# Kernel tuning notes

Measured on AMD Instinct MI355X. Metric: run time of the kernel, lower is better.

## Reference

```python
import jax, jax.numpy as jnp
import numpy as np

N = 100000        # nodes
E_RAND = 1600000  # random edges (self loops appended -> E = E_RAND + N)
H = 64            # agg_hidden
IN = 7            # in_channels
L = 3             # n_layer
FC = 128          # fc_hidden
C = 2             # num_classes
G = 256           # graphs in the batch
SLOPE = 0.2       # GATv2 LeakyReLU negative slope


def _gatv2(x, src, dst, Wl, bl, Wr, br, att, bias):
    # GATv2Conv, heads=1, concat=True, no edge_attr
    xl = x @ Wl.T + bl                                      # [N,H] source transform
    xr = x @ Wr.T + br                                      # [N,H] target transform
    e = jax.nn.leaky_relu(xl[src] + xr[dst], SLOPE) @ att   # [E] per-edge score
    m = jax.ops.segment_max(e, dst, num_segments=N)         # segment softmax over in-edges
    w = jnp.exp(e - m[dst])
    denom = jax.ops.segment_sum(w, dst, num_segments=N)
    alpha = w / denom[dst]                                  # self loops guarantee denom > 0
    out = jax.ops.segment_sum(alpha[:, None] * xl[src], dst, num_segments=N)
    return out + bias


def _forward(x, eps, m0, v0, mrest, vrest, fc1_W, fc1_b, fc2_W, fc2_b, edge_index, batch):
    src, dst = edge_index[0], edge_index[1]
    mean = jax.nn.elu(_gatv2(x, src, dst, *m0))
    log_var = jax.nn.elu(_gatv2(x, src, dst, *v0))
    for i in range(L - 1):  # dropout is a no-op in eval mode
        mean = jax.nn.elu(_gatv2(mean, src, dst, *[p[i] for p in mrest]))
        log_var = jax.nn.elu(_gatv2(log_var, src, dst, *[p[i] for p in vrest]))
    z = mean + eps * jnp.exp(0.5 * log_var)                 # reparameterize
    counts = jax.ops.segment_sum(jnp.ones((N,), z.dtype), batch, num_segments=G)
    zg = jax.ops.segment_sum(z, batch, num_segments=G) / counts[:, None]  # global_mean_pool
    h = jax.nn.relu(zg @ fc1_W.T + fc1_b)
    logits = h @ fc2_W.T + fc2_b
    return jax.nn.log_softmax(logits, axis=1), mean, log_var


def setup_inputs() -> dict:
    key = jax.random.key(0)
    ks = iter(jax.random.split(key, 48))

    def nrm(shape, s=0.1):
        return s * jax.random.normal(next(ks), shape, jnp.float32)

    x = jax.random.normal(next(ks), (N, IN), jnp.float32)
    src = jax.random.randint(next(ks), (E_RAND,), 0, N)
    dst = jax.random.randint(next(ks), (E_RAND,), 0, N)
    loops = jnp.arange(N)
    edge_index = jnp.stack([jnp.concatenate([src, loops]),
                            jnp.concatenate([dst, loops])])  # add_self_loops=True
    batch = jnp.sort(jax.random.randint(next(ks), (N,), 0, G))
    eps = jax.random.normal(next(ks), (N, H), jnp.float32)

    d = dict(x=x, eps=eps, edge_index=edge_index, batch=batch)
    for pre, din in (("m0", IN), ("v0", IN)):
        d[pre + "_Wl"] = nrm((H, din)); d[pre + "_bl"] = nrm((H,))
        d[pre + "_Wr"] = nrm((H, din)); d[pre + "_br"] = nrm((H,))
        d[pre + "_att"] = nrm((H,));    d[pre + "_bias"] = nrm((H,))
    for pre in ("m", "v"):  # stacked hidden layers [L-1, ...]
        d[pre + "_Wl"] = nrm((L - 1, H, H)); d[pre + "_bl"] = nrm((L - 1, H))
        d[pre + "_Wr"] = nrm((L - 1, H, H)); d[pre + "_br"] = nrm((L - 1, H))
        d[pre + "_att"] = nrm((L - 1, H));   d[pre + "_bias"] = nrm((L - 1, H))
    d["fc1_W"] = nrm((FC, H)); d["fc1_b"] = nrm((FC,))
    d["fc2_W"] = nrm((C, FC)); d["fc2_b"] = nrm((C,))
    return d


def reference(x, eps, edge_index, batch,
              m0_Wl, m0_bl, m0_Wr, m0_br, m0_att, m0_bias,
              v0_Wl, v0_bl, v0_Wr, v0_br, v0_att, v0_bias,
              m_Wl, m_bl, m_Wr, m_br, m_att, m_bias,
              v_Wl, v_bl, v_Wr, v_br, v_att, v_bias,
              fc1_W, fc1_b, fc2_W, fc2_b):
    m0 = (m0_Wl, m0_bl, m0_Wr, m0_br, m0_att, m0_bias)
    v0 = (v0_Wl, v0_bl, v0_Wr, v0_br, v0_att, v0_bias)
    mrest = (m_Wl, m_bl, m_Wr, m_br, m_att, m_bias)
    vrest = (v_Wl, v_bl, v_Wr, v_br, v_att, v_bias)
    return _forward(x, eps, m0, v0, mrest, vrest, fc1_W, fc1_b, fc2_W, fc2_b, edge_index, batch)
```

## Files before the change

### kernel.cpp

```cpp
#include <hip/hip_runtime.h>
#include <hip/hip_fp16.h>
#include <math.h>


#define BSH 7
#define BMSK ((1 << BSH) - 1)
#define CHUNK 4096
#define SNB 4096

typedef _Float16 h2 __attribute__((ext_vector_type(2)));
typedef _Float16 h8 __attribute__((ext_vector_type(8)));
typedef float f4 __attribute__((ext_vector_type(4)));

__device__ __forceinline__ float elu1(float v) {
    return v > 0.f ? v : (__expf(v) - 1.f);
}

__device__ __forceinline__ float exp2fast(float x) {
#if defined(__has_builtin)
#if __has_builtin(__builtin_amdgcn_exp2f)
    return __builtin_amdgcn_exp2f(x);
#else
    return exp2f(x);
#endif
#else
    return exp2f(x);
#endif
}

__device__ __forceinline__ float dot2f(h2 a, h2 b, float c) {
#if defined(__has_builtin)
#if __has_builtin(__builtin_amdgcn_fdot2)
    return __builtin_amdgcn_fdot2(a, b, c, false);
#else
    return fmaf((float)a.x, (float)b.x, fmaf((float)a.y, (float)b.y, c));
#endif
#else
    return fmaf((float)a.x, (float)b.x, fmaf((float)a.y, (float)b.y, c));
#endif
}

template <int CTRL>
__device__ __forceinline__ float dppf(float v) {
    int r = __builtin_amdgcn_update_dpp(0, __builtin_bit_cast(int, v), CTRL, 0xF, 0xF, true);
    return __builtin_bit_cast(float, r);
}


__global__ void k_hist_bucket(const int* __restrict__ dst, int E,
                              int* __restrict__ bcnt, int nbk) {
    __shared__ int h[1024];
    for (int i = threadIdx.x; i < 1024; i += blockDim.x) h[i] = 0;
    __syncthreads();
    int stride = gridDim.x * blockDim.x;
    for (int e = blockIdx.x * blockDim.x + threadIdx.x; e < E; e += stride)
        atomicAdd(&h[dst[e] >> BSH], 1);
    __syncthreads();
    for (int i = threadIdx.x; i < nbk; i += blockDim.x)
        if (h[i]) atomicAdd(&bcnt[i], h[i]);
}

__global__ void k_scan_buckets(const int* __restrict__ bcnt, int nbk, int* __restrict__ boff,
                               int* __restrict__ bfill, int* __restrict__ bin_cnt) {
    __shared__ int sh[1024];
    int t = threadIdx.x;
    if (t < nbk) bfill[t] = 0;
    if (t < 256) bin_cnt[t] = 0;
    int v = (t < nbk) ? bcnt[t] : 0;
    sh[t] = v;
    __syncthreads();
    for (int o = 1; o < 1024; o <<= 1) {
        int u = (t >= o) ? sh[t - o] : 0;
        __syncthreads();
        sh[t] += u;
        __syncthreads();
    }
    if (t < nbk) boff[t] = sh[t] - v;
    if (t == nbk - 1) boff[nbk] = sh[t];
}

__global__ __launch_bounds__(256) void k_binfill(
    const int* __restrict__ src, const int* __restrict__ dst, int E,
    const int* __restrict__ boff, int* __restrict__ bfill, int* __restrict__ pairs) {
    __shared__ int h[1024];
    __shared__ int sbase[1024];
    int c0 = blockIdx.x * CHUNK;
    int c1 = min(c0 + CHUNK, E);
    for (int i = threadIdx.x; i < 1024; i += 256) h[i] = 0;
    __syncthreads();
    for (int e = c0 + threadIdx.x; e < c1; e += 256)
        atomicAdd(&h[dst[e] >> BSH], 1);
    __syncthreads();
    for (int i = threadIdx.x; i < 1024; i += 256) {
        int c = h[i];
        sbase[i] = c ? (boff[i] + atomicAdd(&bfill[i], c)) : 0;
        h[i] = 0;
    }
    __syncthreads();
    for (int e = c0 + threadIdx.x; e < c1; e += 256) {
        int d = dst[e];
        int b = d >> BSH;
        int off = atomicAdd(&h[b], 1);
        pairs[sbase[b] + off] = (src[e] << BSH) | (d & BMSK);
    }
}

__global__ __launch_bounds__(256) void k_bucket_csr(
    const int* __restrict__ pairs, const int* __restrict__ boff,
    int* __restrict__ rowptr, int* __restrict__ col, int N, int E) {
    __shared__ int deg[128], fill[128], scan[128], base[128];
    int b = blockIdx.x;
    int e0 = boff[b], e1 = boff[b + 1];
    int t = threadIdx.x;
    if (t < 128) { deg[t] = 0; fill[t] = 0; }
    __syncthreads();
    for (int i = e0 + t; i < e1; i += 256)
        atomicAdd(&deg[pairs[i] & BMSK], 1);
    __syncthreads();
    if (t < 128) scan[t] = deg[t];
    __syncthreads();
    for (int o = 1; o < 128; o <<= 1) {
        int u = (t >= o && t < 128) ? scan[t - o] : 0;
        __syncthreads();
        if (t < 128) scan[t] += u;
        __syncthreads();
    }
    if (t < 128) {
        int excl = e0 + scan[t] - deg[t];
        int node = (b << BSH) + t;
        if (node < N) rowptr[node] = excl;
        if (node == N - 1) rowptr[N] = E;
        base[t] = excl;
    }
    __syncthreads();
    for (int i = e0 + t; i < e1; i += 256) {
        int pk = pairs[i];
        int d = pk & BMSK;
        int pos = base[d] + atomicAdd(&fill[d], 1);
        col[pos] = ((unsigned)pk) >> BSH;
    }
}


__global__ __launch_bounds__(256) void k_deg_hist(const int* __restrict__ rowptr, int n,
                                                  int* __restrict__ bin_cnt,
                                                  int* __restrict__ blk_base) {
    __shared__ int h[256];
    h[threadIdx.x] = 0;
    __syncthreads();
    int b0 = blockIdx.x * SNB;
    int b1 = min(b0 + SNB, n);
    for (int i = b0 + threadIdx.x; i < b1; i += 256) {
        int d = 255 - min(rowptr[i + 1] - rowptr[i], 255);
        atomicAdd(&h[d], 1);
    }
    __syncthreads();
    int c = h[threadIdx.x];
    blk_base[blockIdx.x * 256 + threadIdx.x] = c ? atomicAdd(&bin_cnt[threadIdx.x], c) : 0;
}

__global__ void k_scan256(const int* __restrict__ bin_cnt, int* __restrict__ bin_off,
                          float* __restrict__ zsum, int G) {
    __shared__ int sh[256];
    int t = threadIdx.x;
    for (int i = t; i < G * 64; i += 256) zsum[i] = 0.f;
    int v = bin_cnt[t];
    sh[t] = v;
    __syncthreads();
    for (int o = 1; o < 256; o <<= 1) {
        int u = (t >= o) ? sh[t - o] : 0;
        __syncthreads();
        sh[t] += u;
        __syncthreads();
    }
    bin_off[t] = sh[t] - v;
}

__global__ __launch_bounds__(256) void k_deg_scatter(const int* __restrict__ rowptr, int n,
                                                     const int* __restrict__ bin_off,
                                                     const int* __restrict__ blk_base,
                                                     int* __restrict__ nodeof) {
    __shared__ int h[256];
    h[threadIdx.x] = 0;
    __syncthreads();
    int b0 = blockIdx.x * SNB;
    int b1 = min(b0 + SNB, n);
    for (int i = b0 + threadIdx.x; i < b1; i += 256) {
        int d = 255 - min(rowptr[i + 1] - rowptr[i], 255);
        int my = atomicAdd(&h[d], 1);
        nodeof[bin_off[d] + blk_base[blockIdx.x * 256 + d] + my] = i;
    }
}


__global__ void k_transform7(const float* __restrict__ X,
                             const float* __restrict__ mWl, const float* __restrict__ mbl,
                             const float* __restrict__ mWr, const float* __restrict__ mbr,
                             const float* __restrict__ vWl, const float* __restrict__ vbl,
                             const float* __restrict__ vWr, const float* __restrict__ vbr,
                             __half* __restrict__ xlb, __half* __restrict__ xrb, int n) {
    int t = blockIdx.x * blockDim.x + threadIdx.x;
    int node = t >> 6;
    if (node >= n) return;
    int h = t & 63;
    float aml = mbl[h], amr = mbr[h], avl = vbl[h], avr = vbr[h];
#pragma unroll
    for (int k = 0; k < 7; ++k) {
        float xv = X[node * 7 + k];
        aml = fmaf(xv, mWl[h * 7 + k], aml);
        amr = fmaf(xv, mWr[h * 7 + k], amr);
        avl = fmaf(xv, vWl[h * 7 + k], avl);
        avr = fmaf(xv, vWr[h * 7 + k], avr);
    }
    size_t o = (size_t)node * 128;
    xlb[o + h] = __float2half(aml);
    xlb[o + 64 + h] = __float2half(avl);
    xrb[o + h] = __float2half(amr);
    xrb[o + 64 + h] = __float2half(avr);
}

__global__ __launch_bounds__(256) void k_transform_mfma2(
    const __half* __restrict__ Xm, const __half* __restrict__ Xv,
    const float* __restrict__ mWl, const float* __restrict__ mbl,
    const float* __restrict__ mWr, const float* __restrict__ mbr,
    const float* __restrict__ vWl, const float* __restrict__ vbl,
    const float* __restrict__ vWr, const float* __restrict__ vbr,
    __half* __restrict__ xlb, __half* __restrict__ xrb, int n) {
    int brn = blockIdx.y;
    const __half* X = brn ? Xv : Xm;
    const float* Wl = brn ? vWl : mWl;
    const float* bl = brn ? vbl : mbl;
    const float* Wr = brn ? vWr : mWr;
    const float* br = brn ? vbr : mbr;
    int base = brn * 64;

    __shared__ float biasLds[128];
    {
        int t = threadIdx.x;
        if (t < 64) biasLds[t] = bl[t];
        else if (t < 128) biasLds[t] = br[t - 64];
    }
    __syncthreads();
    int lane = threadIdx.x & 63;
    int l16 = lane & 15, lhi = lane >> 4;

    h8 aW[2][8];
    const float* Wp0 = Wl + (size_t)l16 * 64 + lhi * 8;
    const float* Wp1 = Wr + (size_t)l16 * 64 + lhi * 8;
#pragma unroll
    for (int tl = 0; tl < 4; ++tl) {
#pragma unroll
        for (int c = 0; c < 2; ++c) {
            const float* p0 = Wp0 + (size_t)tl * 16 * 64 + c * 32;
            const float* p1 = Wp1 + (size_t)tl * 16 * 64 + c * 32;
            float4 u0 = *(const float4*)p0, u1 = *(const float4*)(p0 + 4);
            float4 v0 = *(const float4*)p1, v1 = *(const float4*)(p1 + 4);
            h8 a0 = {(_Float16)u0.x, (_Float16)u0.y, (_Float16)u0.z, (_Float16)u0.w,
                     (_Float16)u1.x, (_Float16)u1.y, (_Float16)u1.z, (_Float16)u1.w};
            h8 a1 = {(_Float16)v0.x, (_Float16)v0.y, (_Float16)v0.z, (_Float16)v0.w,
                     (_Float16)v1.x, (_Float16)v1.y, (_Float16)v1.z, (_Float16)v1.w};
            aW[0][tl * 2 + c] = a0;
            aW[1][tl * 2 + c] = a1;
        }
    }

    int ntiles = (n + 15) >> 4;
    int wtile = blockIdx.x * 4 + (threadIdx.x >> 6);
    int wstride = gridDim.x * 4;
    for (int tile = wtile; tile < ntiles; tile += wstride) {
        int nb = tile * 16;
        int node = nb + l16;
        int nload = min(node, n - 1);
        h8 Bf[2];
#pragma unroll
        for (int c = 0; c < 2; ++c) {
            const __half* p = X + (size_t)nload * 64 + c * 32 + lhi * 8;
            Bf[c] = *(const h8*)p;
        }
        f4 acc[2][4];
#pragma unroll
        for (int m = 0; m < 2; ++m)
#pragma unroll
            for (int tl = 0; tl < 4; ++tl) {
                f4 a = {0.f, 0.f, 0.f, 0.f};
                a = __builtin_amdgcn_mfma_f32_16x16x32_f16(aW[m][tl * 2 + 0], Bf[0], a, 0, 0, 0);
                a = __builtin_amdgcn_mfma_f32_16x16x32_f16(aW[m][tl * 2 + 1], Bf[1], a, 0, 0, 0);
                acc[m][tl] = a;
            }
        if (node < n) {
#pragma unroll
            for (int m = 0; m < 2; ++m) {
                __half* op = (m ? xrb : xlb) + (size_t)node * 128 + base;
#pragma unroll
                for (int tl = 0; tl < 4; ++tl) {
                    float4 bb = *(const float4*)&biasLds[m * 64 + tl * 16 + 4 * lhi];
                    h2 lo = {(_Float16)(acc[m][tl][0] + bb.x), (_Float16)(acc[m][tl][1] + bb.y)};
                    h2 hi = {(_Float16)(acc[m][tl][2] + bb.z), (_Float16)(acc[m][tl][3] + bb.w)};
                    uint2 pk = {*(unsigned*)&lo, *(unsigned*)&hi};
                    *(uint2*)(op + tl * 16 + 4 * lhi) = pk;
                }
            }
        }
    }
}


template <bool HOUT>
__global__ __launch_bounds__(256) void k_aggregate2(
    const __half* __restrict__ xlb, const __half* __restrict__ xrb,
    const float* __restrict__ attm, const float* __restrict__ attv,
    const float* __restrict__ biasm, const float* __restrict__ biasv,
    const int* __restrict__ rowptr, const int* __restrict__ col,
    const int* __restrict__ nodeof,
    void* __restrict__ outm, void* __restrict__ outv, int n) {
    int t = blockIdx.x * blockDim.x + threadIdx.x;
    int gid = t >> 4;
    if (gid >= n) return;
    int node = nodeof[gid];
    int l = t & 15;
    int s = l & 7;
    bool isv = l >= 8;

    int4 xri = ((const int4*)(xrb + (size_t)node * 128))[l];
    h2 xr0 = *(h2*)&xri.x, xr1 = *(h2*)&xri.y, xr2 = *(h2*)&xri.z, xr3 = *(h2*)&xri.w;
    const float* ap = (isv ? attv : attm) + s * 8;
    float4 af0 = *(const float4*)ap, af1 = *(const float4*)(ap + 4);
    const float C6 = 0.6f * 1.44269504f;
    const float C4 = 0.4f * 1.44269504f;
    h2 a6_0 = {(_Float16)(af0.x * C6), (_Float16)(af0.y * C6)};
    h2 a6_1 = {(_Float16)(af0.z * C6), (_Float16)(af0.w * C6)};
    h2 a6_2 = {(_Float16)(af1.x * C6), (_Float16)(af1.y * C6)};
    h2 a6_3 = {(_Float16)(af1.z * C6), (_Float16)(af1.w * C6)};
    h2 a4_0 = {(_Float16)(af0.x * C4), (_Float16)(af0.y * C4)};
    h2 a4_1 = {(_Float16)(af0.z * C4), (_Float16)(af0.w * C4)};
    h2 a4_2 = {(_Float16)(af1.x * C4), (_Float16)(af1.y * C4)};
    h2 a4_3 = {(_Float16)(af1.z * C4), (_Float16)(af1.w * C4)};

    float ac0 = 0.f, ac1 = 0.f, ac2 = 0.f, ac3 = 0.f;
    float ac4 = 0.f, ac5 = 0.f, ac6 = 0.f, ac7 = 0.f;
    float ssum = 0.f;

    auto proc = [&](int4 qi) {
        h2 x0 = *(h2*)&qi.x, x1 = *(h2*)&qi.y, x2 = *(h2*)&qi.z, x3 = *(h2*)&qi.w;
        h2 y0 = x0 + xr0, y1 = x1 + xr1, y2 = x2 + xr2, y3 = x3 + xr3;
        int z0i = (*(int*)&y0) & 0x7FFF7FFF;
        int z1i = (*(int*)&y1) & 0x7FFF7FFF;
        int z2i = (*(int*)&y2) & 0x7FFF7FFF;
        int z3i = (*(int*)&y3) & 0x7FFF7FFF;
        h2 z0 = *(h2*)&z0i, z1 = *(h2*)&z1i, z2 = *(h2*)&z2i, z3 = *(h2*)&z3i;
        float sc = dot2f(y0, a6_0, 0.f);
        float sa = dot2f(z0, a4_0, 0.f);
        sc = dot2f(y1, a6_1, sc);
        sa = dot2f(z1, a4_1, sa);
        sc = dot2f(y2, a6_2, sc);
        sa = dot2f(z2, a4_2, sa);
        sc = dot2f(y3, a6_3, sc);
        sa = dot2f(z3, a4_3, sa);
        sc += sa;
        sc += dppf<0xB1>(sc);
        sc += dppf<0x4E>(sc);
        sc += dppf<0x141>(sc);
        float w = exp2fast(sc);
        ssum += w;
        ac0 = fmaf(w, (float)x0.x, ac0);
        ac1 = fmaf(w, (float)x0.y, ac1);
        ac2 = fmaf(w, (float)x1.x, ac2);
        ac3 = fmaf(w, (float)x1.y, ac3);
        ac4 = fmaf(w, (float)x2.x, ac4);
        ac5 = fmaf(w, (float)x2.y, ac5);
        ac6 = fmaf(w, (float)x3.x, ac6);
        ac7 = fmaf(w, (float)x3.y, ac7);
    };

    int r0 = rowptr[node], r1 = rowptr[node + 1];
    const int4* xp = (const int4*)xlb + l;
    int last = r1 - 1;
    int nb = (r1 - r0) >> 2;
    int e = r0;
    int t0 = 0, t1 = 0, t2 = 0, t3 = 0;
    int4 qA0, qA1, qA2, qA3;
    if (nb) {
        int s0 = col[e], s1 = col[e + 1], s2 = col[e + 2], s3 = col[e + 3];
        qA0 = xp[(size_t)s0 * 16]; qA1 = xp[(size_t)s1 * 16];
        qA2 = xp[(size_t)s2 * 16]; qA3 = xp[(size_t)s3 * 16];
        int p = e + 4;
        t0 = col[min(p, last)];     t1 = col[min(p + 1, last)];
        t2 = col[min(p + 2, last)]; t3 = col[min(p + 3, last)];
    }
    for (int b = 0; b < nb; ++b) {
        int4 qB0, qB1, qB2, qB3;
        bool more = (b + 1 < nb);
        if (more) {
            qB0 = xp[(size_t)t0 * 16]; qB1 = xp[(size_t)t1 * 16];
            qB2 = xp[(size_t)t2 * 16]; qB3 = xp[(size_t)t3 * 16];
            int p = e + 8;
            t0 = col[min(p, last)];     t1 = col[min(p + 1, last)];
            t2 = col[min(p + 2, last)]; t3 = col[min(p + 3, last)];
        }
        proc(qA0); proc(qA1); proc(qA2); proc(qA3);
        if (more) { qA0 = qB0; qA1 = qB1; qA2 = qB2; qA3 = qB3; }
        e += 4;
    }
    for (e = r0 + nb * 4; e < r1; ++e)
        proc(xp[(size_t)col[e] * 16]);

    float inv = 1.f / ssum;
    const float* bp = (isv ? biasv : biasm) + s * 8;
    float4 b0 = *(const float4*)bp, b1 = *(const float4*)(bp + 4);
    float r00 = elu1(fmaf(ac0, inv, b0.x));
    float r01 = elu1(fmaf(ac1, inv, b0.y));
    float r02 = elu1(fmaf(ac2, inv, b0.z));
    float r03 = elu1(fmaf(ac3, inv, b0.w));
    float r04 = elu1(fmaf(ac4, inv, b1.x));
    float r05 = elu1(fmaf(ac5, inv, b1.y));
    float r06 = elu1(fmaf(ac6, inv, b1.z));
    float r07 = elu1(fmaf(ac7, inv, b1.w));
    if (HOUT) {
        __half* op = (__half*)(isv ? outv : outm) + (size_t)node * 64 + s * 8;
        h2 p0 = {(_Float16)r00, (_Float16)r01}, p1 = {(_Float16)r02, (_Float16)r03};
        h2 p2 = {(_Float16)r04, (_Float16)r05}, p3 = {(_Float16)r06, (_Float16)r07};
        uint4 pk = {*(unsigned*)&p0, *(unsigned*)&p1, *(unsigned*)&p2, *(unsigned*)&p3};
        *(uint4*)op = pk;
    } else {
        float* op = (float*)(isv ? outv : outm) + (size_t)node * 64 + s * 8;
        float4 r0v = {r00, r01, r02, r03};
        float4 r1v = {r04, r05, r06, r07};
        *(float4*)op = r0v;
        *(float4*)(op + 4) = r1v;
    }
}


__global__ void k_zpool(const float* __restrict__ mean, const float* __restrict__ logvar,
                        const float* __restrict__ eps, const int* __restrict__ batch,
                        float* __restrict__ zsum, int n) {
    int wave = blockIdx.x * 4 + (threadIdx.x >> 6);
    int lane = threadIdx.x & 63;
    int n0 = wave * 16;
    if (n0 >= n) return;
    int n1 = min(n0 + 16, n);
    float acc = 0.f;
    int gcur = -1;
    for (int nd = n0; nd < n1; ++nd) {
        int g = batch[nd];
        if (g != gcur) {
            if (gcur >= 0) atomicAdd(&zsum[gcur * 64 + lane], acc);
            gcur = g; acc = 0.f;
        }
        size_t o = (size_t)nd * 64 + lane;
        acc += fmaf(eps[o], __expf(0.5f * logvar[o]), mean[o]);
    }
    if (gcur >= 0) atomicAdd(&zsum[gcur * 64 + lane], acc);
}


__global__ void k_fchead(const float* __restrict__ zsum, const int* __restrict__ batch,
                         int N,
                         const float* __restrict__ fc1W, const float* __restrict__ fc1b,
                         const float* __restrict__ fc2W, const float* __restrict__ fc2b,
                         float* __restrict__ out) {
    __shared__ float zg[64];
    __shared__ float h1[128];
    __shared__ float lg[2];
    __shared__ int bnd[2];
    int g = blockIdx.x;
    int t = threadIdx.x;
    if (t < 2) {
        int tgt = g + t, lo = 0, hi = N;
        while (lo < hi) {
            int m = (lo + hi) >> 1;
            if (batch[m] < tgt) lo = m + 1; else hi = m;
        }
        bnd[t] = lo;
    }
    __syncthreads();
    float cntg = (float)(bnd[1] - bnd[0]);
    if (t < 64) zg[t] = zsum[g * 64 + t] / cntg;
    __syncthreads();
    float h = fc1b[t];
#pragma unroll
    for (int k = 0; k < 64; ++k) h = fmaf(zg[k], fc1W[t * 64 + k], h);
    h1[t] = fmaxf(h, 0.f);
    __syncthreads();
    if (t < 2) {
        float l = fc2b[t];
        for (int k = 0; k < 128; ++k) l = fmaf(h1[k], fc2W[t * 128 + k], l);
        lg[t] = l;
    }
    __syncthreads();
    if (t == 0) {
        float mx = fmaxf(lg[0], lg[1]);
        float lse = mx + logf(expf(lg[0] - mx) + expf(lg[1] - mx));
        out[g * 2 + 0] = lg[0] - lse;
        out[g * 2 + 1] = lg[1] - lse;
    }
}


extern "C" void kernel_launch(void* const* d_in, const int* in_sizes, int n_in,
                              void* d_out, int out_size, void* d_ws, size_t ws_size,
                              hipStream_t stream) {
    const float* x     = (const float*)d_in[0];
    const float* eps   = (const float*)d_in[1];
    const int*   eidx  = (const int*)d_in[2];
    const int*   batch = (const int*)d_in[3];
    const float* m0_Wl = (const float*)d_in[4];
    const float* m0_bl = (const float*)d_in[5];
    const float* m0_Wr = (const float*)d_in[6];
    const float* m0_br = (const float*)d_in[7];
    const float* m0_att = (const float*)d_in[8];
    const float* m0_bias = (const float*)d_in[9];
    const float* v0_Wl = (const float*)d_in[10];
    const float* v0_bl = (const float*)d_in[11];
    const float* v0_Wr = (const float*)d_in[12];
    const float* v0_br = (const float*)d_in[13];
    const float* v0_att = (const float*)d_in[14];
    const float* v0_bias = (const float*)d_in[15];
    const float* m_Wl = (const float*)d_in[16];
    const float* m_bl = (const float*)d_in[17];
    const float* m_Wr = (const float*)d_in[18];
    const float* m_br = (const float*)d_in[19];
    const float* m_att = (const float*)d_in[20];
    const float* m_bias = (const float*)d_in[21];
    const float* v_Wl = (const float*)d_in[22];
    const float* v_bl = (const float*)d_in[23];
    const float* v_Wr = (const float*)d_in[24];
    const float* v_br = (const float*)d_in[25];
    const float* v_att = (const float*)d_in[26];
    const float* v_bias = (const float*)d_in[27];
    const float* fc1W = (const float*)d_in[28];
    const float* fc1b = (const float*)d_in[29];
    const float* fc2W = (const float*)d_in[30];
    const float* fc2b = (const float*)d_in[31];

    const int N = in_sizes[1] / 64;
    const int E = in_sizes[2] / 2;
    const int G = (out_size - N * 128) / 2;
    const int nbk = (N + (1 << BSH) - 1) >> BSH;
    const int nsb = (N + SNB - 1) / SNB;
    const int* srcp = eidx;
    const int* dstp = eidx + E;

    char* wsb = (char*)d_ws;
    size_t off = 0;
    auto carve = [&](size_t bytes) -> void* {
        void* p = wsb + off;
        off += (bytes + 255) & ~(size_t)255;
        return p;
    };
    int*    rowptr   = (int*)carve((size_t)(N + 1) * sizeof(int));
    int*    col      = (int*)carve((size_t)E * sizeof(int));
    int*    pairs    = (int*)carve((size_t)E * sizeof(int));
    int*    bcnt     = (int*)carve((size_t)(nbk + 1) * sizeof(int));
    int*    boff     = (int*)carve((size_t)(nbk + 1) * sizeof(int));
    int*    bfill    = (int*)carve((size_t)nbk * sizeof(int));
    int*    nodeof   = (int*)carve((size_t)N * sizeof(int));
    int*    bin_cnt  = (int*)carve(256 * sizeof(int));
    int*    bin_off  = (int*)carve(256 * sizeof(int));
    int*    blk_base = (int*)carve((size_t)nsb * 256 * sizeof(int));
    __half* xlb      = (__half*)carve((size_t)N * 128 * sizeof(__half));
    __half* xrb      = (__half*)carve((size_t)N * 128 * sizeof(__half));
    __half* meanh    = (__half*)carve((size_t)N * 64 * sizeof(__half));
    __half* logvarh  = (__half*)carve((size_t)N * 64 * sizeof(__half));
    float*  zsum     = (float*)carve((size_t)G * 64 * sizeof(float));
    (void)ws_size;

    float* out_logits = (float*)d_out;
    float* mean_buf   = out_logits + (size_t)G * 2;
    float* logvar_buf = mean_buf + (size_t)N * 64;

    const int agrid = (N * 16 + 255) / 256;
    const int tgrid7 = (N * 64 + 255) / 256;
    const int ntiles = (N + 15) / 16;
    const int mgrid = (ntiles + 15) / 16;
    const int zgrid = ((N + 15) / 16 + 3) / 4;

    (void)hipMemsetAsync(bcnt, 0, (size_t)nbk * sizeof(int), stream);
    k_hist_bucket<<<256, 256, 0, stream>>>(dstp, E, bcnt, nbk);
    k_scan_buckets<<<1, 1024, 0, stream>>>(bcnt, nbk, boff, bfill, bin_cnt);
    k_binfill<<<(E + CHUNK - 1) / CHUNK, 256, 0, stream>>>(srcp, dstp, E, boff, bfill, pairs);
    k_bucket_csr<<<nbk, 256, 0, stream>>>(pairs, boff, rowptr, col, N, E);

    k_deg_hist<<<nsb, 256, 0, stream>>>(rowptr, N, bin_cnt, blk_base);
    k_scan256<<<1, 256, 0, stream>>>(bin_cnt, bin_off, zsum, G);
    k_deg_scatter<<<nsb, 256, 0, stream>>>(rowptr, N, bin_off, blk_base, nodeof);

    k_transform7<<<tgrid7, 256, 0, stream>>>(x, m0_Wl, m0_bl, m0_Wr, m0_br,
                                             v0_Wl, v0_bl, v0_Wr, v0_br, xlb, xrb, N);
    k_aggregate2<true><<<agrid, 256, 0, stream>>>(
        xlb, xrb, m0_att, v0_att, m0_bias, v0_bias,
        rowptr, col, nodeof, meanh, logvarh, N);

    for (int l = 0; l < 2; ++l) {
        k_transform_mfma2<<<dim3(mgrid, 2), 256, 0, stream>>>(
            meanh, logvarh,
            m_Wl + (size_t)l * 4096, m_bl + l * 64, m_Wr + (size_t)l * 4096, m_br + l * 64,
            v_Wl + (size_t)l * 4096, v_bl + l * 64, v_Wr + (size_t)l * 4096, v_br + l * 64,
            xlb, xrb, N);
        if (l == 0)
            k_aggregate2<true><<<agrid, 256, 0, stream>>>(
                xlb, xrb, m_att + l * 64, v_att + l * 64, m_bias + l * 64, v_bias + l * 64,
                rowptr, col, nodeof, meanh, logvarh, N);
        else
            k_aggregate2<false><<<agrid, 256, 0, stream>>>(
                xlb, xrb, m_att + l * 64, v_att + l * 64, m_bias + l * 64, v_bias + l * 64,
                rowptr, col, nodeof, mean_buf, logvar_buf, N);
    }

    k_zpool<<<zgrid, 256, 0, stream>>>(mean_buf, logvar_buf, eps, batch, zsum, N);
    k_fchead<<<G, 128, 0, stream>>>(zsum, batch, N, fc1W, fc1b, fc2W, fc2b, out_logits);
}
```

Before: 406.7 us.

## Fuse degree scatter into first transform, widen transform7 stores, prefetch MFMA tiles

The degree-bucket scatter that builds nodeof is folded into the first k_transform7 launch, with the first nsb blocks doing the scatter before their transform work, which removes one kernel launch. k_transform7 now gives each thread two output channels and writes packed half2 values, halving the thread count and widening the stores. k_transform_mfma2 software-prefetches the next tile's input fragment before running the MFMAs on the current tile, to overlap the global load with compute. The fused blocks carry extra scatter work, which can make those blocks stragglers in the launch.

```diff
diff --git a/kernel.cpp b/kernel.cpp
--- a/kernel.cpp
+++ b/kernel.cpp
@@ -176,47 +176,57 @@
     bin_off[t] = sh[t] - v;
 }
 
-__global__ __launch_bounds__(256) void k_deg_scatter(const int* __restrict__ rowptr, int n,
-                                                     const int* __restrict__ bin_off,
-                                                     const int* __restrict__ blk_base,
-                                                     int* __restrict__ nodeof) {
-    __shared__ int h[256];
-    h[threadIdx.x] = 0;
-    __syncthreads();
-    int b0 = blockIdx.x * SNB;
-    int b1 = min(b0 + SNB, n);
-    for (int i = b0 + threadIdx.x; i < b1; i += 256) {
-        int d = 255 - min(rowptr[i + 1] - rowptr[i], 255);
-        int my = atomicAdd(&h[d], 1);
-        nodeof[bin_off[d] + blk_base[blockIdx.x * 256 + d] + my] = i;
-    }
-}
-
-
-__global__ void k_transform7(const float* __restrict__ X,
-                             const float* __restrict__ mWl, const float* __restrict__ mbl,
-                             const float* __restrict__ mWr, const float* __restrict__ mbr,
-                             const float* __restrict__ vWl, const float* __restrict__ vbl,
-                             const float* __restrict__ vWr, const float* __restrict__ vbr,
-                             __half* __restrict__ xlb, __half* __restrict__ xrb, int n) {
+
+__global__ __launch_bounds__(256) void k_transform7(
+    const float* __restrict__ X,
+    const float* __restrict__ mWl, const float* __restrict__ mbl,
+    const float* __restrict__ mWr, const float* __restrict__ mbr,
+    const float* __restrict__ vWl, const float* __restrict__ vbl,
+    const float* __restrict__ vWr, const float* __restrict__ vbr,
+    __half* __restrict__ xlb, __half* __restrict__ xrb, int n,
+    const int* __restrict__ rowptr, const int* __restrict__ bin_off,
+    const int* __restrict__ blk_base, int* __restrict__ nodeof, int nsb) {
+    if (blockIdx.x < (unsigned)nsb) {
+        __shared__ int h[256];
+        h[threadIdx.x] = 0;
+        __syncthreads();
+        int b0 = blockIdx.x * SNB;
+        int b1 = min(b0 + SNB, n);
+        for (int i = b0 + threadIdx.x; i < b1; i += 256) {
+            int d = 255 - min(rowptr[i + 1] - rowptr[i], 255);
+            int my = atomicAdd(&h[d], 1);
+            nodeof[bin_off[d] + blk_base[blockIdx.x * 256 + d] + my] = i;
+        }
+    }
     int t = blockIdx.x * blockDim.x + threadIdx.x;
-    int node = t >> 6;
+    int node = t >> 5;
     if (node >= n) return;
-    int h = t & 63;
-    float aml = mbl[h], amr = mbr[h], avl = vbl[h], avr = vbr[h];
+    int c2 = (t & 31) * 2;
+    float aml0 = mbl[c2], aml1 = mbl[c2 + 1];
+    float amr0 = mbr[c2], amr1 = mbr[c2 + 1];
+    float avl0 = vbl[c2], avl1 = vbl[c2 + 1];
+    float avr0 = vbr[c2], avr1 = vbr[c2 + 1];
 #pragma unroll
     for (int k = 0; k < 7; ++k) {
         float xv = X[node * 7 + k];
-        aml = fmaf(xv, mWl[h * 7 + k], aml);
-        amr = fmaf(xv, mWr[h * 7 + k], amr);
-        avl = fmaf(xv, vWl[h * 7 + k], avl);
-        avr = fmaf(xv, vWr[h * 7 + k], avr);
+        aml0 = fmaf(xv, mWl[c2 * 7 + k], aml0);
+        aml1 = fmaf(xv, mWl[(c2 + 1) * 7 + k], aml1);
+        amr0 = fmaf(xv, mWr[c2 * 7 + k], amr0);
+        amr1 = fmaf(xv, mWr[(c2 + 1) * 7 + k], amr1);
+        avl0 = fmaf(xv, vWl[c2 * 7 + k], avl0);
+        avl1 = fmaf(xv, vWl[(c2 + 1) * 7 + k], avl1);
+        avr0 = fmaf(xv, vWr[c2 * 7 + k], avr0);
+        avr1 = fmaf(xv, vWr[(c2 + 1) * 7 + k], avr1);
     }
     size_t o = (size_t)node * 128;
-    xlb[o + h] = __float2half(aml);
-    xlb[o + 64 + h] = __float2half(avl);
-    xrb[o + h] = __float2half(amr);
-    xrb[o + 64 + h] = __float2half(avr);
+    h2 pml = {(_Float16)aml0, (_Float16)aml1};
+    h2 pvl = {(_Float16)avl0, (_Float16)avl1};
+    h2 pmr = {(_Float16)amr0, (_Float16)amr1};
+    h2 pvr = {(_Float16)avr0, (_Float16)avr1};
+    *(h2*)(xlb + o + c2) = pml;
+    *(h2*)(xlb + o + 64 + c2) = pvl;
+    *(h2*)(xrb + o + c2) = pmr;
+    *(h2*)(xrb + o + 64 + c2) = pvr;
 }
 
 __global__ __launch_bounds__(256) void k_transform_mfma2(
@@ -265,17 +275,23 @@
     }
 
     int ntiles = (n + 15) >> 4;
-    int wtile = blockIdx.x * 4 + (threadIdx.x >> 6);
     int wstride = gridDim.x * 4;
-    for (int tile = wtile; tile < ntiles; tile += wstride) {
-        int nb = tile * 16;
-        int node = nb + l16;
-        int nload = min(node, n - 1);
-        h8 Bf[2];
-#pragma unroll
-        for (int c = 0; c < 2; ++c) {
-            const __half* p = X + (size_t)nload * 64 + c * 32 + lhi * 8;
-            Bf[c] = *(const h8*)p;
+    int tile = blockIdx.x * 4 + (threadIdx.x >> 6);
+    h8 Bf[2];
+    if (tile < ntiles) {
+        int nload = min(tile * 16 + l16, n - 1);
+        const __half* p = X + (size_t)nload * 64 + lhi * 8;
+        Bf[0] = *(const h8*)p;
+        Bf[1] = *(const h8*)(p + 32);
+    }
+    for (; tile < ntiles; tile += wstride) {
+        int next = tile + wstride;
+        h8 BfN[2];
+        if (next < ntiles) {
+            int nloadN = min(next * 16 + l16, n - 1);
+            const __half* p = X + (size_t)nloadN * 64 + lhi * 8;
+            BfN[0] = *(const h8*)p;
+            BfN[1] = *(const h8*)(p + 32);
         }
         f4 acc[2][4];
 #pragma unroll
@@ -287,6 +303,7 @@
                 a = __builtin_amdgcn_mfma_f32_16x16x32_f16(aW[m][tl * 2 + 1], Bf[1], a, 0, 0, 0);
                 acc[m][tl] = a;
             }
+        int node = tile * 16 + l16;
         if (node < n) {
 #pragma unroll
             for (int m = 0; m < 2; ++m) {
@@ -301,6 +318,7 @@
                 }
             }
         }
+        if (next < ntiles) { Bf[0] = BfN[0]; Bf[1] = BfN[1]; }
     }
 }
 
@@ -570,7 +588,7 @@
     float* logvar_buf = mean_buf + (size_t)N * 64;
 
     const int agrid = (N * 16 + 255) / 256;
-    const int tgrid7 = (N * 64 + 255) / 256;
+    const int tgrid7 = (N * 32 + 255) / 256;
     const int ntiles = (N + 15) / 16;
     const int mgrid = (ntiles + 15) / 16;
     const int zgrid = ((N + 15) / 16 + 3) / 4;
@@ -583,10 +601,10 @@
 
     k_deg_hist<<<nsb, 256, 0, stream>>>(rowptr, N, bin_cnt, blk_base);
     k_scan256<<<1, 256, 0, stream>>>(bin_cnt, bin_off, zsum, G);
-    k_deg_scatter<<<nsb, 256, 0, stream>>>(rowptr, N, bin_off, blk_base, nodeof);
 
     k_transform7<<<tgrid7, 256, 0, stream>>>(x, m0_Wl, m0_bl, m0_Wr, m0_br,
-                                             v0_Wl, v0_bl, v0_Wr, v0_br, xlb, xrb, N);
+                                             v0_Wl, v0_bl, v0_Wr, v0_br, xlb, xrb, N,
+                                             rowptr, bin_off, blk_base, nodeof, nsb);
     k_aggregate2<true><<<agrid, 256, 0, stream>>>(
         xlb, xrb, m0_att, v0_att, m0_bias, v0_bias,
         rowptr, col, nodeof, meanh, logvarh, N);
```

Measured after the change: 396.5 us. -2.5%, faster.
